# Kernel tuning notes

Measured on AMD Instinct MI355X. Metric: run time of the kernel, lower is better.

## Reference

```python
import jax, jax.numpy as jnp
import numpy as np

N_EMBD = 2048
N_HEAD = 32
N_GROUPS = 8
HEAD_DIM = N_EMBD // N_HEAD
Q_PER_KV = N_HEAD // N_GROUPS
QKV_DIM = (Q_PER_KV + 2) * N_GROUPS * HEAD_DIM


def apply_rope(x, cos, sin):
    # x: [B, nH, T, hd]; cos/sin: [T, rot//2]
    B, nH, T, hd = x.shape
    rot = min(sin.shape[1] * 2, hd)
    half = rot // 2
    x_rot, x_pass = x[..., :rot], x[..., rot:]
    c = cos[:T, :half][None, None]  # [1,1,T,half]
    s = sin[:T, :half][None, None]
    x1, x2 = x_rot[..., :half], x_rot[..., half:]
    x1_ = x1 * c - x2 * s
    x2_ = x2 * c + x1 * s
    return jnp.concatenate([x1_, x2_, x_pass], axis=-1)


def setup_inputs() -> dict:
    key = jax.random.key(0)
    k1, k2, k3, k4, k5 = jax.random.split(key, 5)
    B, T = 2, 2048
    x = jax.random.normal(k1, (B, T, N_EMBD), dtype=jnp.float32)
    cos = jax.random.uniform(k2, (T, HEAD_DIM // 2), dtype=jnp.float32)
    sin = jax.random.uniform(k3, (T, HEAD_DIM // 2), dtype=jnp.float32)
    attn_w = jax.random.normal(k4, (QKV_DIM, N_EMBD), dtype=jnp.float32) * (1.0 / np.sqrt(N_EMBD))
    proj_w = jax.random.normal(k5, (N_EMBD, N_EMBD), dtype=jnp.float32) * (1.0 / np.sqrt(N_EMBD))
    return {"x": x, "cos": cos, "sin": sin, "attn_w": attn_w, "proj_w": proj_w}


def reference(x, cos, sin, attn_w, proj_w):
    B, T, E = x.shape
    qkv = jnp.einsum('bte,fe->btf', x, attn_w)  # [B,T,QKV_DIM]
    qkv = qkv.reshape(B, T, N_GROUPS, Q_PER_KV + 2, HEAD_DIM)
    q = qkv[:, :, :, :Q_PER_KV].reshape(B, T, N_HEAD, HEAD_DIM)
    k = qkv[:, :, :, Q_PER_KV]      # [B,T,G,hd]
    v = qkv[:, :, :, Q_PER_KV + 1]  # [B,T,G,hd]
    # [B, heads, T, hd] layout; GQA repeat_interleave of K/V to full head count
    q = q.transpose(0, 2, 1, 3)
    k = jnp.repeat(k.transpose(0, 2, 1, 3), Q_PER_KV, axis=1)
    v = jnp.repeat(v.transpose(0, 2, 1, 3), Q_PER_KV, axis=1)
    q = apply_rope(q, cos, sin)
    k = apply_rope(k, cos, sin)
    scale = 1.0 / np.sqrt(HEAD_DIM)
    att = jax.nn.softmax(jnp.einsum('bhqd,bhkd->bhqk', q, k) * scale, axis=-1)
    out = jnp.einsum('bhqk,bhkd->bhqd', att, v)  # [B,nH,T,hd]
    out = out.transpose(0, 2, 1, 3).reshape(B, T, N_HEAD * HEAD_DIM)
    return jnp.einsum('bte,fe->btf', out, proj_w)
```

## Files before the change

### kernel.cpp

```cpp
#include <hip/hip_runtime.h>

typedef unsigned short u16;
typedef unsigned int u32;
typedef __bf16 bf16x8 __attribute__((ext_vector_type(8)));
typedef float f32x4 __attribute__((ext_vector_type(4)));
typedef float f32x16 __attribute__((ext_vector_type(16)));
typedef unsigned int u32x4 __attribute__((ext_vector_type(4)));

__device__ __forceinline__ u16 f2bf(float f) {
    u32 u = __builtin_bit_cast(u32, f);
    u32 r = u + 0x7FFFu + ((u >> 16) & 1u);
    return (u16)(r >> 16);
}
__device__ __forceinline__ u32 pack_bf16(float v0, float v1) {
    u32 a = __builtin_bit_cast(u32, v0) + 0x8000u;
    u32 b = __builtin_bit_cast(u32, v1) + 0x8000u;
    return __builtin_amdgcn_perm(b, a, 0x07060302u);
}
__device__ __forceinline__ u32 cvtpk(float lo, float hi) {
    u32 r;
    asm("v_cvt_pk_bf16_f32 %0, %1, %2" : "=v"(r) : "v"(lo), "v"(hi));
    return r;
}
__device__ __forceinline__ void plswap(u32& a, u32& b) {
    asm("v_permlane32_swap_b32 %0, %1" : "+v"(a), "+v"(b));
}
__device__ __forceinline__ void gload16(const u16* g, u16* l) {
    __builtin_amdgcn_global_load_lds(
        (const __attribute__((address_space(1))) u32*)g,
        (__attribute__((address_space(3))) u32*)l, 16, 0, 0);
}

#define QSCALE 0.18033688011111793f


__global__ __launch_bounds__(256) void cvt3_kernel(const float* __restrict__ a, u16* __restrict__ ao,
                                                   const float* __restrict__ b, u16* __restrict__ bo,
                                                   const float* __restrict__ c, u16* __restrict__ co) {
    int i = blockIdx.x * 256 + threadIdx.x;
    const float* src; u16* dst; int idx;
    if (i < 2097152)       { src = a; dst = ao; idx = i; }
    else if (i < 3670016)  { src = b; dst = bo; idx = i - 2097152; }
    else                   { src = c; dst = co; idx = i - 3670016; }
    float4 f = reinterpret_cast<const float4*>(src)[idx];
    u32 lo = (u32)f2bf(f.x) | ((u32)f2bf(f.y) << 16);
    u32 hi = (u32)f2bf(f.z) | ((u32)f2bf(f.w) << 16);
    reinterpret_cast<uint2*>(dst)[idx] = make_uint2(lo, hi);
}

__global__ __launch_bounds__(512, 2) void gemm_qkv(const u16* __restrict__ A,
                                                   const u16* __restrict__ Bw,
                                                   const float* __restrict__ cosb,
                                                   const float* __restrict__ sinb,
                                                   u16* __restrict__ Qo,
                                                   u16* __restrict__ Ko,
                                                   u16* __restrict__ Vt) {
    __shared__ __align__(16) u16 As[2 * 128 * 64];
    __shared__ __align__(16) u16 Bs[2 * 384 * 64];
    const int tid = threadIdx.x;
    const int w = tid >> 6, lane = tid & 63;
    const int quad = lane >> 4, l15 = lane & 15;
    const int wr = w >> 1, wc = w & 1;
    const int m0 = blockIdx.x * 128, n0 = blockIdx.y * 384;
    const int K = 2048;
    const int rsub = lane >> 3;
    const int csrc = (lane & 7) ^ rsub;
    const int sx = (l15 & 7) << 3;
    const int c0 = (quad * 8) ^ sx;
    const int c1 = (32 + quad * 8) ^ sx;

    f32x4 acc[2][12];
#pragma unroll
    for (int a = 0; a < 2; a++)
#pragma unroll
        for (int b = 0; b < 12; b++) acc[a][b] = (f32x4){0.f, 0.f, 0.f, 0.f};

    auto stageA = [&](int kk, u16* lds) {
#pragma unroll
        for (int i = 0; i < 2; i++)
            gload16(A + (size_t)(m0 + (i * 8 + w) * 8 + rsub) * K + kk + csrc * 8,
                    lds + (i * 8 + w) * 512);
    };
    auto stageB = [&](int kk, u16* lds, int hf) {
#pragma unroll
        for (int i = 0; i < 3; i++) {
            const int grp = hf * 24 + i * 8 + w;
            gload16(Bw + (size_t)(n0 + grp * 8 + rsub) * K + kk + csrc * 8,
                    lds + grp * 512);
        }
    };

    stageA(0, &As[0]);
    stageB(0, &Bs[0], 0);
    stageB(0, &Bs[0], 1);
    asm volatile("s_waitcnt vmcnt(0)" ::: "memory");
    __builtin_amdgcn_s_barrier();

    for (int j = 0; j < 32; ++j) {
        const int cur = j & 1;
        const u16* Ab = &As[cur * 8192];
        const u16* Bb = &Bs[cur * 24576];
        u16* Asn = &As[(cur ^ 1) * 8192];
        u16* Bsn = &Bs[(cur ^ 1) * 24576];
        const int kk2 = (j + 1) * 64;
        bf16x8 af[2][2];
#pragma unroll
        for (int ph = 0; ph < 2; ++ph) {
            if (ph == 0) {
#pragma unroll
                for (int fm = 0; fm < 2; fm++) {
                    const int r = wr * 32 + fm * 16 + l15;
                    af[fm][0] = *reinterpret_cast<const bf16x8*>(&Ab[r * 64 + c0]);
                    af[fm][1] = *reinterpret_cast<const bf16x8*>(&Ab[r * 64 + c1]);
                }
            }
            bf16x8 bfv[6][2];
#pragma unroll
            for (int fn = 0; fn < 6; fn++) {
                const int nr = wc * 192 + ph * 96 + fn * 16 + l15;
                bfv[fn][0] = *reinterpret_cast<const bf16x8*>(&Bb[nr * 64 + c0]);
                bfv[fn][1] = *reinterpret_cast<const bf16x8*>(&Bb[nr * 64 + c1]);
            }
            if (j < 31) {
                if (ph == 0) { stageA(kk2, Asn); stageB(kk2, Bsn, 0); }
                else         stageB(kk2, Bsn, 1);
            }
            __builtin_amdgcn_s_barrier();
            __builtin_amdgcn_s_setprio(1);
#pragma unroll
            for (int fm = 0; fm < 2; fm++)
#pragma unroll
                for (int fn = 0; fn < 6; fn++) {
                    acc[fm][ph * 6 + fn] = __builtin_amdgcn_mfma_f32_16x16x32_bf16(
                        af[fm][0], bfv[fn][0], acc[fm][ph * 6 + fn], 0, 0, 0);
                    acc[fm][ph * 6 + fn] = __builtin_amdgcn_mfma_f32_16x16x32_bf16(
                        af[fm][1], bfv[fn][1], acc[fm][ph * 6 + fn], 0, 0, 0);
                }
            __builtin_amdgcn_s_setprio(0);
            if (ph == 1 && j < 31) asm volatile("s_waitcnt vmcnt(0)" ::: "memory");
            __builtin_amdgcn_s_barrier();
        }
    }

    const int G = blockIdx.y;
    const int bb = m0 >> 11;
    const int tb0 = (m0 & 2047) + wr * 32 + quad * 4;
    const int laneoff = (l15 >> 3) * 256 + (l15 & 7);
    u16* vbase = Vt + ((size_t)(bb * 8 + G)) * 131072;
#pragma unroll
    for (int fn = 0; fn < 12; fn++) {
        const int slotf = wc * 3 + (fn >> 2);
        const int f = fn & 3;
        if (slotf == 5) {
#pragma unroll
            for (int fm = 0; fm < 2; fm++) {
                const int trow = tb0 + fm * 16;
                const int sb = (trow >> 6) * 4096 + ((trow >> 4) & 3) * 512
                             + (quad >> 1) * 256 + (quad & 1) * 4;
                uint2 pk;
                pk.x = pack_bf16(acc[fm][fn][0], acc[fm][fn][1]);
                pk.y = pack_bf16(acc[fm][fn][2], acc[fm][fn][3]);
                *reinterpret_cast<uint2*>(vbase + sb + (f >> 1) * 2048
                                          + ((f & 1) * 16 + l15) * 8) = pk;
            }
        } else if (f < 2) {
            const float sc = (slotf < 4) ? QSCALE : 1.0f;
            u16* obase = (slotf < 4)
                ? Qo + ((size_t)(bb * 32 + G * 4 + slotf)) * 131072
                : Ko + ((size_t)(bb * 8 + G)) * 131072;
#pragma unroll
            for (int fm = 0; fm < 2; fm++)
#pragma unroll
                for (int i = 0; i < 4; i++) {
                    const int t = tb0 + fm * 16 + i;
                    const int tb = (t >> 5) * 2048 + (t & 31) * 8 + laneoff;
                    const int dh = f * 16 + l15;
                    float c = cosb[t * 32 + dh], s = sinb[t * 32 + dh];
                    float x1 = acc[fm][fn][i], x2 = acc[fm][fn + 2][i];
                    obase[tb + f * 512]       = f2bf((x1 * c - x2 * s) * sc);
                    obase[tb + (f + 2) * 512] = f2bf((x2 * c + x1 * s) * sc);
                }
        }
    }
}

__global__ __launch_bounds__(512, 2) void gemm_bt(const u16* __restrict__ A,
                                                  const u16* __restrict__ Bw,
                                                  float* __restrict__ Cf,
                                                  int M, int N, int K) {
    __shared__ __align__(16) u16 As[2 * 128 * 64];
    __shared__ __align__(16) u16 Bs[2 * 2 * 128 * 64];
    const int tid = threadIdx.x;
    const int w = tid >> 6, lane = tid & 63;
    const int quad = lane >> 4, l15 = lane & 15;
    const int wr = w >> 2, wc = w & 3;
    const int m0 = blockIdx.x * 128, n0 = blockIdx.y * 256;
    const int rsub = lane >> 3;
    const int csrc = (lane & 7) ^ rsub;
    const int sx = (l15 & 7) << 3;
    const int c0 = (quad * 8) ^ sx;
    const int c1 = (32 + quad * 8) ^ sx;

    f32x4 acc[4][4];
#pragma unroll
    for (int a = 0; a < 4; a++)
#pragma unroll
        for (int b = 0; b < 4; b++) acc[a][b] = (f32x4){0.f, 0.f, 0.f, 0.f};

    auto stage = [&](const u16* g, int row0, int kk, u16* lds) {
#pragma unroll
        for (int i = 0; i < 2; i++)
            gload16(g + (size_t)(row0 + (i * 8 + w) * 8 + rsub) * K + kk + csrc * 8,
                    lds + (i * 8 + w) * 512);
    };

    stage(A,  m0,       0, &As[0]);
    stage(Bw, n0,       0, &Bs[0]);
    stage(Bw, n0 + 128, 0, &Bs[8192]);
    asm volatile("s_waitcnt vmcnt(0)" ::: "memory");
    __builtin_amdgcn_s_barrier();

    const int nt = K >> 6;
    for (int j = 0; j < nt; ++j) {
        const int cur = j & 1;
        const u16* Ab = &As[cur * 8192];
        const u16* Bb = &Bs[cur * 16384 + (wc >> 1) * 8192 + (wc & 1) * 4096];
        u16* Asn = &As[(cur ^ 1) * 8192];
        u16* Bsn = &Bs[(cur ^ 1) * 16384];
        const int kk2 = (j + 1) * 64;
        bf16x8 af[4][2];
#pragma unroll
        for (int ph = 0; ph < 2; ++ph) {
            if (ph == 0) {
#pragma unroll
                for (int fm = 0; fm < 4; fm++) {
                    const int r = wr * 64 + fm * 16 + l15;
                    af[fm][0] = *reinterpret_cast<const bf16x8*>(&Ab[r * 64 + c0]);
                    af[fm][1] = *reinterpret_cast<const bf16x8*>(&Ab[r * 64 + c1]);
                }
            }
            bf16x8 bfv[2][2];
#pragma unroll
            for (int fn = 0; fn < 2; fn++) {
                const int nr = (ph * 2 + fn) * 16 + l15;
                bfv[fn][0] = *reinterpret_cast<const bf16x8*>(&Bb[nr * 64 + c0]);
                bfv[fn][1] = *reinterpret_cast<const bf16x8*>(&Bb[nr * 64 + c1]);
            }
            if (j < nt - 1) {
                if (ph == 0) { stage(A, m0, kk2, Asn); stage(Bw, n0, kk2, Bsn); }
                else         stage(Bw, n0 + 128, kk2, Bsn + 8192);
            }
            __builtin_amdgcn_s_barrier();
            __builtin_amdgcn_s_setprio(1);
#pragma unroll
            for (int fm = 0; fm < 4; fm++)
#pragma unroll
                for (int fn = 0; fn < 2; fn++) {
                    acc[fm][ph * 2 + fn] = __builtin_amdgcn_mfma_f32_16x16x32_bf16(
                        af[fm][0], bfv[fn][0], acc[fm][ph * 2 + fn], 0, 0, 0);
                    acc[fm][ph * 2 + fn] = __builtin_amdgcn_mfma_f32_16x16x32_bf16(
                        af[fm][1], bfv[fn][1], acc[fm][ph * 2 + fn], 0, 0, 0);
                }
            __builtin_amdgcn_s_setprio(0);
            if (ph == 1 && j < nt - 1) asm volatile("s_waitcnt vmcnt(0)" ::: "memory");
            __builtin_amdgcn_s_barrier();
        }
    }

#pragma unroll
    for (int tm = 0; tm < 4; tm++) {
        const int r0 = m0 + wr * 64 + tm * 16 + quad * 4;
#pragma unroll
        for (int tn = 0; tn < 4; tn++) {
            const int c = n0 + wc * 64 + tn * 16 + l15;
#pragma unroll
            for (int i = 0; i < 4; i++) Cf[(size_t)(r0 + i) * N + c] = acc[tm][tn][i];
        }
    }
}

__global__ __launch_bounds__(256, 4) void attn(const u16* __restrict__ Q,
                                               const u16* __restrict__ Kg,
                                               const u16* __restrict__ Vt,
                                               u16* __restrict__ O) {
    __shared__ __align__(16) u16 Ks[3 * 4096];
    __shared__ __align__(16) u16 Vts[2 * 4096];
    const int tid = threadIdx.x, w = tid >> 6, lane = tid & 63;
    const int half = lane >> 5, l31 = lane & 31;
    const int q0 = blockIdx.x * 128;
    const int h = blockIdx.y, b = blockIdx.z, g = h >> 2;
    const u16* qfb = Q + ((size_t)(b * 32 + h)) * 131072;
    const u16* kfb = Kg + ((size_t)(b * 8 + g)) * 131072;
    const u16* vfb = Vt + ((size_t)(b * 8 + g)) * 131072;

    const int Tq = (q0 >> 6) + (w >> 1);
#pragma unroll
    for (int ks = 0; ks < 4; ks++)
        gload16(qfb + ((size_t)((Tq * 8 + (w & 1) * 4 + ks) * 64) + lane) * 8,
                Ks + (w * 4 + ks) * 512);
    __syncthreads();
    bf16x8 qf[4];
#pragma unroll
    for (int ks = 0; ks < 4; ks++)
        qf[ks] = *reinterpret_cast<const bf16x8*>(&Ks[(w * 4 + ks) * 512 + lane * 8]);
    __syncthreads();

    f32x16 Oa[2];
#pragma unroll
    for (int t = 0; t < 2; t++)
#pragma unroll
        for (int i = 0; i < 16; i++) Oa[t][i] = 0.f;
    float lsum = 0.f;

    auto stage_k = [&](int T, int bsel) {
        u16* kd = Ks + bsel * 4096;
#pragma unroll
        for (int i = 0; i < 2; i++) {
            const int s = w * 2 + i;
            gload16(kfb + ((size_t)((T * 8 + s) * 64) + lane) * 8, kd + s * 512);
        }
    };
    auto stage_v = [&](int T, int bsel) {
        u16* vd = Vts + bsel * 4096;
#pragma unroll
        for (int i = 0; i < 2; i++) {
            const int s = w * 2 + i;
            gload16(vfb + ((size_t)((T * 8 + s) * 64) + lane) * 8, vd + s * 512);
        }
    };
    auto qk = [&](f32x16 (&S)[2], const u16* Kb) {
#pragma unroll
        for (int kt = 0; kt < 2; kt++) {
#pragma unroll
            for (int i = 0; i < 16; i++) S[kt][i] = 0.f;
#pragma unroll
            for (int ks = 0; ks < 4; ks++) {
                bf16x8 kf = *reinterpret_cast<const bf16x8*>(&Kb[(kt * 4 + ks) * 512 + lane * 8]);
                S[kt] = __builtin_amdgcn_mfma_f32_32x32x16_bf16(kf, qf[ks], S[kt], 0, 0, 0);
            }
        }
    };

    stage_k(0, 0);
    stage_v(0, 0);
    stage_k(1, 1);
    __syncthreads();
    f32x16 Sa[2], Sb[2];
    __builtin_amdgcn_s_setprio(1);
    qk(Sa, Ks);
    __builtin_amdgcn_s_setprio(0);

    auto body = [&](int t, int bn, int bs, f32x16 (&Sc)[2], f32x16 (&Sn)[2],
                    const u16* Vb) {
        if (t < 31) stage_v(t + 1, (t + 1) & 1);
        if (t < 30) stage_k(t + 2, bs);
        float ps = 0.f;
        u32 pw[4][4];
#pragma unroll
        for (int kt = 0; kt < 2; kt++) {
            float pe[16];
#pragma unroll
            for (int r = 0; r < 16; r++) pe[r] = __builtin_amdgcn_exp2f(Sc[kt][r]);
#pragma unroll
            for (int r = 0; r < 4; r++)
                ps += (pe[r * 4 + 0] + pe[r * 4 + 1]) + (pe[r * 4 + 2] + pe[r * 4 + 3]);
#pragma unroll
            for (int j = 0; j < 2; j++) {
                u32 X0 = cvtpk(pe[j * 8 + 0], pe[j * 8 + 1]);
                u32 Y0 = cvtpk(pe[j * 8 + 4], pe[j * 8 + 5]);
                u32 X1 = cvtpk(pe[j * 8 + 2], pe[j * 8 + 3]);
                u32 Y1 = cvtpk(pe[j * 8 + 6], pe[j * 8 + 7]);
                plswap(X0, Y0);
                plswap(X1, Y1);
                const int ks2 = kt * 2 + j;
                pw[ks2][0] = X0; pw[ks2][1] = X1; pw[ks2][2] = Y0; pw[ks2][3] = Y1;
            }
        }
        __builtin_amdgcn_s_setprio(1);
        qk(Sn, Ks + bn * 4096);
#pragma unroll
        for (int ks2 = 0; ks2 < 4; ks2++) {
            u32x4 pv = (u32x4){pw[ks2][0], pw[ks2][1], pw[ks2][2], pw[ks2][3]};
            bf16x8 pf = __builtin_bit_cast(bf16x8, pv);
#pragma unroll
            for (int dt = 0; dt < 2; dt++) {
                bf16x8 vf = *reinterpret_cast<const bf16x8*>(
                    &Vb[(dt * 4 + ks2) * 512 + lane * 8]);
                Oa[dt] = __builtin_amdgcn_mfma_f32_32x32x16_bf16(vf, pf, Oa[dt], 0, 0, 0);
            }
        }
        __builtin_amdgcn_s_setprio(0);
        lsum += ps;
        __syncthreads();
    };

    int b0 = 0, b1 = 1, b2 = 2;
    for (int k2 = 0; k2 < 16; ++k2) {
        const int t0 = k2 * 2;
        body(t0,     b1, b2, Sa, Sb, Vts);
        body(t0 + 1, b2, b0, Sb, Sa, Vts + 4096);
        const int nb0 = b2, nb1 = b0, nb2 = b1;
        b0 = nb0; b1 = nb1; b2 = nb2;
    }

    float lt = lsum + __shfl_xor(lsum, 32);
    float linv = 1.f / lt;
    const int t = q0 + w * 32 + l31;
    u16* orow = O + ((size_t)(b * 2048 + t)) * 2048 + h * 64;
#pragma unroll
    for (int dt = 0; dt < 2; dt++)
#pragma unroll
        for (int gr = 0; gr < 4; gr++) {
            uint2 pk;
            pk.x = pack_bf16(Oa[dt][gr * 4 + 0] * linv, Oa[dt][gr * 4 + 1] * linv);
            pk.y = pack_bf16(Oa[dt][gr * 4 + 2] * linv, Oa[dt][gr * 4 + 3] * linv);
            *reinterpret_cast<uint2*>(orow + dt * 32 + 8 * gr + 4 * half) = pk;
        }
}

extern "C" void kernel_launch(void* const* d_in, const int* in_sizes, int n_in,
                              void* d_out, int out_size, void* d_ws, size_t ws_size,
                              hipStream_t stream) {
    const float* x      = (const float*)d_in[0];
    const float* cosb   = (const float*)d_in[1];
    const float* sinb   = (const float*)d_in[2];
    const float* attn_w = (const float*)d_in[3];
    const float* proj_w = (const float*)d_in[4];
    float* out = (float*)d_out;

    u16* xb  = (u16*)d_ws;
    u16* w1b = xb  + (size_t)4096 * 2048;
    u16* w2b = w1b + (size_t)3072 * 2048;
    u16* qo  = w2b + (size_t)2048 * 2048;
    u16* ko  = qo  + (size_t)2 * 32 * 2048 * 64;
    u16* vt  = ko  + (size_t)2 * 8 * 2048 * 64;
    u16* ao  = xb;

    cvt3_kernel<<<18432, 256, 0, stream>>>(x, xb, attn_w, w1b, proj_w, w2b);
    gemm_qkv<<<dim3(32, 8), 512, 0, stream>>>(xb, w1b, cosb, sinb, qo, ko, vt);
    attn<<<dim3(16, 32, 2), 256, 0, stream>>>(qo, ko, vt, ao);
    gemm_bt<<<dim3(32, 8), 512, 0, stream>>>(ao, w2b, out, 4096, 2048, 2048);
}
```

Baseline: 291.6 us.

## Process two query tiles per wave in attention to reuse K/V fragments

Each attention wave now handles 64 query rows (two 32-row tiles) instead of 32. This doubles reuse of every K and V fragment read from shared memory and halves the grid. The triple-buffered, software-pipelined QK/PV schedule is replaced by a simple double-buffered loop that stages K and V together. The costs are higher register pressure (launch bound drops to 2 blocks per CU), fewer blocks, and the loss of the overlap between the next tile's QK and the current tile's PV.

```diff
diff --git a/kernel.cpp b/kernel.cpp
--- a/kernel.cpp
+++ b/kernel.cpp
@@ -279,143 +279,139 @@
     }
 }
 
-__global__ __launch_bounds__(256, 4) void attn(const u16* __restrict__ Q,
+__global__ __launch_bounds__(256, 2) void attn(const u16* __restrict__ Q,
                                                const u16* __restrict__ Kg,
                                                const u16* __restrict__ Vt,
                                                u16* __restrict__ O) {
-    __shared__ __align__(16) u16 Ks[3 * 4096];
+    __shared__ __align__(16) u16 Ks[2 * 4096];
     __shared__ __align__(16) u16 Vts[2 * 4096];
     const int tid = threadIdx.x, w = tid >> 6, lane = tid & 63;
     const int half = lane >> 5, l31 = lane & 31;
-    const int q0 = blockIdx.x * 128;
+    const int q0 = blockIdx.x * 256;
     const int h = blockIdx.y, b = blockIdx.z, g = h >> 2;
     const u16* qfb = Q + ((size_t)(b * 32 + h)) * 131072;
     const u16* kfb = Kg + ((size_t)(b * 8 + g)) * 131072;
     const u16* vfb = Vt + ((size_t)(b * 8 + g)) * 131072;
 
-    const int Tq = (q0 >> 6) + (w >> 1);
-#pragma unroll
-    for (int ks = 0; ks < 4; ks++)
-        gload16(qfb + ((size_t)((Tq * 8 + (w & 1) * 4 + ks) * 64) + lane) * 8,
-                Ks + (w * 4 + ks) * 512);
+    const int Tq = (q0 >> 6) + w;
+    u16* qs = (w < 2 ? Ks : Vts) + (w & 1) * 4096;
+#pragma unroll
+    for (int s = 0; s < 8; s++)
+        gload16(qfb + ((size_t)((Tq * 8 + s) * 64) + lane) * 8, qs + s * 512);
     __syncthreads();
-    bf16x8 qf[4];
-#pragma unroll
-    for (int ks = 0; ks < 4; ks++)
-        qf[ks] = *reinterpret_cast<const bf16x8*>(&Ks[(w * 4 + ks) * 512 + lane * 8]);
+    bf16x8 qf[2][4];
+#pragma unroll
+    for (int qa = 0; qa < 2; qa++)
+#pragma unroll
+        for (int ks = 0; ks < 4; ks++)
+            qf[qa][ks] = *reinterpret_cast<const bf16x8*>(&qs[(qa * 4 + ks) * 512 + lane * 8]);
     __syncthreads();
 
-    f32x16 Oa[2];
-#pragma unroll
-    for (int t = 0; t < 2; t++)
-#pragma unroll
-        for (int i = 0; i < 16; i++) Oa[t][i] = 0.f;
-    float lsum = 0.f;
-
-    auto stage_k = [&](int T, int bsel) {
+    f32x16 Oa[2][2];
+#pragma unroll
+    for (int qa = 0; qa < 2; qa++)
+#pragma unroll
+        for (int dt = 0; dt < 2; dt++)
+#pragma unroll
+            for (int i = 0; i < 16; i++) Oa[qa][dt][i] = 0.f;
+    float lsum0 = 0.f, lsum1 = 0.f;
+
+    auto stage_kv = [&](int T, int bsel) {
         u16* kd = Ks + bsel * 4096;
+        u16* vd = Vts + bsel * 4096;
 #pragma unroll
         for (int i = 0; i < 2; i++) {
             const int s = w * 2 + i;
             gload16(kfb + ((size_t)((T * 8 + s) * 64) + lane) * 8, kd + s * 512);
+            gload16(vfb + ((size_t)((T * 8 + s) * 64) + lane) * 8, vd + s * 512);
         }
     };
-    auto stage_v = [&](int T, int bsel) {
-        u16* vd = Vts + bsel * 4096;
-#pragma unroll
-        for (int i = 0; i < 2; i++) {
-            const int s = w * 2 + i;
-            gload16(vfb + ((size_t)((T * 8 + s) * 64) + lane) * 8, vd + s * 512);
-        }
-    };
-    auto qk = [&](f32x16 (&S)[2], const u16* Kb) {
+
+    stage_kv(0, 0);
+    __syncthreads();
+
+    for (int t = 0; t < 32; t++) {
+        if (t < 31) stage_kv(t + 1, (t + 1) & 1);
+        const u16* Kb = Ks + (t & 1) * 4096;
+        const u16* Vb = Vts + (t & 1) * 4096;
+
+        float ps0 = 0.f, ps1 = 0.f;
+        u32 pw0[4][4], pw1[4][4];
 #pragma unroll
         for (int kt = 0; kt < 2; kt++) {
-#pragma unroll
-            for (int i = 0; i < 16; i++) S[kt][i] = 0.f;
-#pragma unroll
-            for (int ks = 0; ks < 4; ks++) {
-                bf16x8 kf = *reinterpret_cast<const bf16x8*>(&Kb[(kt * 4 + ks) * 512 + lane * 8]);
-                S[kt] = __builtin_amdgcn_mfma_f32_32x32x16_bf16(kf, qf[ks], S[kt], 0, 0, 0);
-            }
-        }
-    };
-
-    stage_k(0, 0);
-    stage_v(0, 0);
-    stage_k(1, 1);
-    __syncthreads();
-    f32x16 Sa[2], Sb[2];
-    __builtin_amdgcn_s_setprio(1);
-    qk(Sa, Ks);
-    __builtin_amdgcn_s_setprio(0);
-
-    auto body = [&](int t, int bn, int bs, f32x16 (&Sc)[2], f32x16 (&Sn)[2],
-                    const u16* Vb) {
-        if (t < 31) stage_v(t + 1, (t + 1) & 1);
-        if (t < 30) stage_k(t + 2, bs);
-        float ps = 0.f;
-        u32 pw[4][4];
-#pragma unroll
-        for (int kt = 0; kt < 2; kt++) {
-            float pe[16];
-#pragma unroll
-            for (int r = 0; r < 16; r++) pe[r] = __builtin_amdgcn_exp2f(Sc[kt][r]);
-#pragma unroll
-            for (int r = 0; r < 4; r++)
-                ps += (pe[r * 4 + 0] + pe[r * 4 + 1]) + (pe[r * 4 + 2] + pe[r * 4 + 3]);
-#pragma unroll
-            for (int j = 0; j < 2; j++) {
-                u32 X0 = cvtpk(pe[j * 8 + 0], pe[j * 8 + 1]);
-                u32 Y0 = cvtpk(pe[j * 8 + 4], pe[j * 8 + 5]);
-                u32 X1 = cvtpk(pe[j * 8 + 2], pe[j * 8 + 3]);
-                u32 Y1 = cvtpk(pe[j * 8 + 6], pe[j * 8 + 7]);
-                plswap(X0, Y0);
-                plswap(X1, Y1);
-                const int ks2 = kt * 2 + j;
-                pw[ks2][0] = X0; pw[ks2][1] = X1; pw[ks2][2] = Y0; pw[ks2][3] = Y1;
-            }
-        }
+            bf16x8 kf[4];
+#pragma unroll
+            for (int ks = 0; ks < 4; ks++)
+                kf[ks] = *reinterpret_cast<const bf16x8*>(&Kb[(kt * 4 + ks) * 512 + lane * 8]);
+#pragma unroll
+            for (int qa = 0; qa < 2; qa++) {
+                f32x16 S;
+#pragma unroll
+                for (int i = 0; i < 16; i++) S[i] = 0.f;
+                __builtin_amdgcn_s_setprio(1);
+#pragma unroll
+                for (int ks = 0; ks < 4; ks++)
+                    S = __builtin_amdgcn_mfma_f32_32x32x16_bf16(kf[ks], qf[qa][ks], S, 0, 0, 0);
+                __builtin_amdgcn_s_setprio(0);
+                float pe[16];
+#pragma unroll
+                for (int r = 0; r < 16; r++) pe[r] = __builtin_amdgcn_exp2f(S[r]);
+                float psl = 0.f;
+#pragma unroll
+                for (int r = 0; r < 4; r++)
+                    psl += (pe[r * 4 + 0] + pe[r * 4 + 1]) + (pe[r * 4 + 2] + pe[r * 4 + 3]);
+                if (qa == 0) ps0 += psl; else ps1 += psl;
+#pragma unroll
+                for (int j = 0; j < 2; j++) {
+                    u32 X0 = cvtpk(pe[j * 8 + 0], pe[j * 8 + 1]);
+                    u32 Y0 = cvtpk(pe[j * 8 + 4], pe[j * 8 + 5]);
+                    u32 X1 = cvtpk(pe[j * 8 + 2], pe[j * 8 + 3]);
+                    u32 Y1 = cvtpk(pe[j * 8 + 6], pe[j * 8 + 7]);
+                    plswap(X0, Y0);
+                    plswap(X1, Y1);
+                    const int ks2 = kt * 2 + j;
+                    if (qa == 0) { pw0[ks2][0] = X0; pw0[ks2][1] = X1; pw0[ks2][2] = Y0; pw0[ks2][3] = Y1; }
+                    else         { pw1[ks2][0] = X0; pw1[ks2][1] = X1; pw1[ks2][2] = Y0; pw1[ks2][3] = Y1; }
+                }
+            }
+        }
+        lsum0 += ps0; lsum1 += ps1;
         __builtin_amdgcn_s_setprio(1);
-        qk(Sn, Ks + bn * 4096);
 #pragma unroll
         for (int ks2 = 0; ks2 < 4; ks2++) {
-            u32x4 pv = (u32x4){pw[ks2][0], pw[ks2][1], pw[ks2][2], pw[ks2][3]};
-            bf16x8 pf = __builtin_bit_cast(bf16x8, pv);
+            u32x4 pv0 = (u32x4){pw0[ks2][0], pw0[ks2][1], pw0[ks2][2], pw0[ks2][3]};
+            u32x4 pv1 = (u32x4){pw1[ks2][0], pw1[ks2][1], pw1[ks2][2], pw1[ks2][3]};
+            bf16x8 pf0 = __builtin_bit_cast(bf16x8, pv0);
+            bf16x8 pf1 = __builtin_bit_cast(bf16x8, pv1);
 #pragma unroll
             for (int dt = 0; dt < 2; dt++) {
                 bf16x8 vf = *reinterpret_cast<const bf16x8*>(
                     &Vb[(dt * 4 + ks2) * 512 + lane * 8]);
-                Oa[dt] = __builtin_amdgcn_mfma_f32_32x32x16_bf16(vf, pf, Oa[dt], 0, 0, 0);
+                Oa[0][dt] = __builtin_amdgcn_mfma_f32_32x32x16_bf16(vf, pf0, Oa[0][dt], 0, 0, 0);
+                Oa[1][dt] = __builtin_amdgcn_mfma_f32_32x32x16_bf16(vf, pf1, Oa[1][dt], 0, 0, 0);
             }
         }
         __builtin_amdgcn_s_setprio(0);
-        lsum += ps;
         __syncthreads();
-    };
-
-    int b0 = 0, b1 = 1, b2 = 2;
-    for (int k2 = 0; k2 < 16; ++k2) {
-        const int t0 = k2 * 2;
-        body(t0,     b1, b2, Sa, Sb, Vts);
-        body(t0 + 1, b2, b0, Sb, Sa, Vts + 4096);
-        const int nb0 = b2, nb1 = b0, nb2 = b1;
-        b0 = nb0; b1 = nb1; b2 = nb2;
-    }
-
-    float lt = lsum + __shfl_xor(lsum, 32);
-    float linv = 1.f / lt;
-    const int t = q0 + w * 32 + l31;
-    u16* orow = O + ((size_t)(b * 2048 + t)) * 2048 + h * 64;
-#pragma unroll
-    for (int dt = 0; dt < 2; dt++)
-#pragma unroll
-        for (int gr = 0; gr < 4; gr++) {
-            uint2 pk;
-            pk.x = pack_bf16(Oa[dt][gr * 4 + 0] * linv, Oa[dt][gr * 4 + 1] * linv);
-            pk.y = pack_bf16(Oa[dt][gr * 4 + 2] * linv, Oa[dt][gr * 4 + 3] * linv);
-            *reinterpret_cast<uint2*>(orow + dt * 32 + 8 * gr + 4 * half) = pk;
-        }
+    }
+
+#pragma unroll
+    for (int qa = 0; qa < 2; qa++) {
+        float ls = (qa == 0) ? lsum0 : lsum1;
+        float lt = ls + __shfl_xor(ls, 32);
+        float linv = 1.f / lt;
+        const int t = q0 + w * 64 + qa * 32 + l31;
+        u16* orow = O + ((size_t)(b * 2048 + t)) * 2048 + h * 64;
+#pragma unroll
+        for (int dt = 0; dt < 2; dt++)
+#pragma unroll
+            for (int gr = 0; gr < 4; gr++) {
+                uint2 pk;
+                pk.x = pack_bf16(Oa[qa][dt][gr * 4 + 0] * linv, Oa[qa][dt][gr * 4 + 1] * linv);
+                pk.y = pack_bf16(Oa[qa][dt][gr * 4 + 2] * linv, Oa[qa][dt][gr * 4 + 3] * linv);
+                *reinterpret_cast<uint2*>(orow + dt * 32 + 8 * gr + 4 * half) = pk;
+            }
+    }
 }
 
 extern "C" void kernel_launch(void* const* d_in, const int* in_sizes, int n_in,
@@ -438,6 +434,6 @@
 
     cvt3_kernel<<<18432, 256, 0, stream>>>(x, xb, attn_w, w1b, proj_w, w2b);
     gemm_qkv<<<dim3(32, 8), 512, 0, stream>>>(xb, w1b, cosb, sinb, qo, ko, vt);
-    attn<<<dim3(16, 32, 2), 256, 0, stream>>>(qo, ko, vt, ao);
+    attn<<<dim3(8, 32, 2), 256, 0, stream>>>(qo, ko, vt, ao);
     gemm_bt<<<dim3(32, 8), 512, 0, stream>>>(ao, w2b, out, 4096, 2048, 2048);
 }
```

After: 287.3 us. No clear change (-1.5%).
